# Performance work log

Hardware: AMD Instinct MI355X
Metric: run time of the kernel (lower is better)

## Reference

```python
import jax, jax.numpy as jnp
import numpy as np

TAU = 2.0          # spikingjelly LIFNode default
V_TH = 7.0         # from source
DECREASE = 0.5     # decrease_factor
ALPHA = 4.0        # sigmoid surrogate alpha (spikingjelly default)


@jax.custom_vjp
def spike(v):
    # Heaviside with sigmoid surrogate gradient
    return (v >= 0.0).astype(v.dtype)

def _spike_fwd(v):
    return spike(v), v

def _spike_bwd(v, g):
    s = jax.nn.sigmoid(ALPHA * v)
    return (g * ALPHA * s * (1.0 - s),)

spike.defvjp(_spike_fwd, _spike_bwd)


def setup_inputs() -> dict:
    key = jax.random.key(0)
    k1, k2, k3 = jax.random.split(key, 3)
    B, C, T = 4096, 14, 600
    x = jax.random.normal(k1, (B, C, T), dtype=jnp.float32)
    # weights: normal(mean=0.8, std=0.05) clamped to [0,1]; nn.Linear stores [out,in]
    W1 = jnp.clip(0.8 + 0.05 * jax.random.normal(k2, (14, 14), dtype=jnp.float32), 0.0, 1.0)
    W2 = jnp.clip(0.8 + 0.05 * jax.random.normal(k3, (500, 14), dtype=jnp.float32), 0.0, 1.0)
    return {"x": x, "W1": W1, "W2": W2}


def _forward(x, W1, W2):
    B = x.shape[0]
    xt = jnp.transpose(x, (2, 0, 1))  # [T, B, 14]

    v1_0 = jnp.zeros((B, 14), x.dtype)
    v2_0 = jnp.zeros((B, 500), x.dtype)
    cache0 = jnp.zeros((B, 14), x.dtype)

    def step(carry, x_t):
        v1, v2, cache = carry
        # block 1: linear + decayed feedback of previous spikes
        i1 = x_t @ W1.T + DECREASE * cache
        v1 = v1 + (i1 - v1) / TAU          # LIF charge (decay_input, v_reset=0)
        s1 = spike(v1 - V_TH)
        v1 = v1 * (1.0 - s1)               # hard reset to 0
        # block 2
        i2 = s1 @ W2.T
        v2 = v2 + (i2 - v2) / TAU
        s2 = spike(v2 - V_TH)
        v2 = v2 * (1.0 - s2)
        return (v1, v2, s1), None

    (v1, v2, cache), _ = jax.lax.scan(step, (v1_0, v2_0, cache0), xt)
    return jnp.exp(v2)  # liquid state [B, 500]


def reference(x, W1, W2):
    return _forward(x, W1, W2)
```

## Files before the change

### kernel.cpp

```cpp
#include <hip/hip_runtime.h>
#include <math.h>

#define T      600
#define C      14
#define NOUT   500
#define R      4
#define W      128
#define DSTR   132
#define EVCAP  256

__global__ __launch_bounds__(128, 2)
void snn_v3(const float* __restrict__ x, const float* __restrict__ W1,
            const float* __restrict__ W2, float* __restrict__ out) {
    __shared__ float    ds[R * C * DSTR];
    __shared__ unsigned evs[R * EVCAP];
    __shared__ int      ecnt[R];

    const int tid = threadIdx.x;
    const int b0  = blockIdx.x * R;
    if (tid < R) ecnt[tid] = 0;

    const int  rr   = tid >> 5;
    const int  qq   = tid & 31;
    const int  cc   = (tid >> 1) & 15;
    const int  ce   = (cc < C) ? cc : (C - 1);
    const bool aact = ((tid & 1) == 0) && (cc < C);

    float4 xv[C];
    #pragma unroll
    for (int j = 0; j < C; ++j)
        xv[j] = *(const float4*)&x[((long)(b0 + rr) * C + j) * T + qq * 4];

    float v1 = 0.f;

    for (int t0 = 0; t0 < T; t0 += W) {
        const int wlen = (T - t0 < W) ? (T - t0) : W;
        __syncthreads();

        if (qq * 4 < wlen) {
            #pragma unroll
            for (int c = 0; c < C; ++c) {
                float ax = 0.f, ay = 0.f, az = 0.f, aw = 0.f;
                #pragma unroll
                for (int j = 0; j < C; ++j) {
                    const float w = 0.5f * W1[c * C + j];
                    ax = fmaf(xv[j].x, w, ax);
                    ay = fmaf(xv[j].y, w, ay);
                    az = fmaf(xv[j].z, w, az);
                    aw = fmaf(xv[j].w, w, aw);
                }
                *(float4*)&ds[(rr * C + c) * DSTR + qq * 4] = make_float4(ax, ay, az, aw);
            }
        }

        {
            const int tn = t0 + W + qq * 4;
            if (tn < T) {
                #pragma unroll
                for (int j = 0; j < C; ++j)
                    xv[j] = *(const float4*)&x[((long)(b0 + rr) * C + j) * T + tn];
            }
        }
        __syncthreads();

        const float* dp = &ds[(rr * C + ce) * DSTR];
        for (int q = 0; q < wlen; q += 4) {
            const float4 hd = *(const float4*)&dp[q];
            const float a  = fmaf(v1, 0.5f, hd.x);
            const float b  = fmaf(a,  0.5f, hd.y);
            const float c2 = fmaf(b,  0.5f, hd.z);
            const float d  = fmaf(c2, 0.5f, hd.w);
            const float m  = fmaxf(fmaxf(a, b), fmaxf(c2, d));
            if (__builtin_expect(__ballot(m >= 7.0f) != 0ull, 0)) {
                float vv = v1;
                #pragma unroll
                for (int u = 0; u < 4; ++u) {
                    const float h = (u == 0) ? hd.x : (u == 1) ? hd.y
                                  : (u == 2) ? hd.z : hd.w;
                    vv = fmaf(vv, 0.5f, h);
                    if (vv >= 7.0f) {
                        vv = 0.5f;
                        if (aact) {
                            const int idx = atomicAdd(&ecnt[rr], 1);
                            if (idx < EVCAP)
                                evs[rr * EVCAP + idx] =
                                    ((unsigned)(t0 + q + u) << 4) | (unsigned)cc;
                        }
                    }
                }
                v1 = vv;
            } else {
                v1 = d;
            }
        }
    }
    __syncthreads();

    const int lane = tid & 31;
    const int nev  = min(ecnt[rr], EVCAP);
    const unsigned* ev = &evs[rr * EVCAP];

    float v2[16];
    #pragma unroll
    for (int k = 0; k < 16; ++k) v2[k] = 0.f;
    int tprev = -1;

    int e = 0;
    while (e < nev) {
        const int t = (int)(ev[e] >> 4);
        float i2[16];
        #pragma unroll
        for (int k = 0; k < 16; ++k) i2[k] = 0.f;
        do {
            const int c = (int)(ev[e] & 15);
            #pragma unroll
            for (int k = 0; k < 16; ++k) {
                const int o = lane + (k << 5);
                if (o < NOUT) i2[k] += W2[o * C + c];
            }
            ++e;
        } while (e < nev && (int)(ev[e] >> 4) == t);

        const int gap = t - tprev - 1;
        if (gap > 0) {
            #pragma unroll
            for (int k = 0; k < 16; ++k) v2[k] = ldexpf(v2[k], -gap);
        }
        #pragma unroll
        for (int k = 0; k < 16; ++k) {
            const float v = v2[k] + (i2[k] - v2[k]) * 0.5f;
            v2[k] = (v >= 7.0f) ? 0.f : v;
        }
        tprev = t;
    }
    {
        const int gap = (T - 1) - tprev;
        if (gap > 0) {
            #pragma unroll
            for (int k = 0; k < 16; ++k) v2[k] = ldexpf(v2[k], -gap);
        }
    }
    #pragma unroll
    for (int k = 0; k < 16; ++k) {
        const int o = lane + (k << 5);
        if (o < NOUT) out[(long)(b0 + rr) * NOUT + o] = expf(v2[k]);
    }
}

extern "C" void kernel_launch(void* const* d_in, const int* in_sizes, int n_in,
                              void* d_out, int out_size, void* d_ws, size_t ws_size,
                              hipStream_t stream) {
    const float* x  = (const float*)d_in[0];
    const float* W1 = (const float*)d_in[1];
    const float* W2 = (const float*)d_in[2];
    float* o = (float*)d_out;
    const int B = in_sizes[0] / (C * T);
    snn_v3<<<B / R, 128, 0, stream>>>(x, W1, W2, o);
}
```

Measured before the change: 44.67 us.

## Split LIF time recurrence into two parallel segments with warm-up overlap

Doubles the block to 256 threads and has each half-block run the first-layer recurrence over a different half of the time axis. The second half starts 32 steps early as a warm-up, relying on the 0.5 decay to wash out the unknown initial membrane state, and records spikes only from step 300 on. The output neurons are also split between the two halves, and each half replays both event lists. This is meant to shorten the serial critical path per block and raise occupancy, at the cost of redundant warm-up work, a per-list event cap cut to 48, and a small risk of state mismatch at the segment boundary.

```diff
diff --git a/kernel.cpp b/kernel.cpp
--- a/kernel.cpp
+++ b/kernel.cpp
@@ -5,144 +5,159 @@
 #define C      14
 #define NOUT   500
 #define R      4
-#define W      128
-#define DSTR   132
-#define EVCAP  256
+#define WW     64
+#define DSTR   68
+#define NW     6
+#define SEG1   268
+#define TMID   300
+#define CAP    48
 
-__global__ __launch_bounds__(128, 2)
-void snn_v3(const float* __restrict__ x, const float* __restrict__ W1,
+__global__ __launch_bounds__(256, 4)
+void snn_v4(const float* __restrict__ x, const float* __restrict__ W1,
             const float* __restrict__ W2, float* __restrict__ out) {
-    __shared__ float    ds[R * C * DSTR];
-    __shared__ unsigned evs[R * EVCAP];
-    __shared__ int      ecnt[R];
+    __shared__ float    ds[2 * R * C * DSTR];
+    __shared__ unsigned evs[2][R][CAP];
+    __shared__ int      ecnt[2][R];
 
     const int tid = threadIdx.x;
     const int b0  = blockIdx.x * R;
-    if (tid < R) ecnt[tid] = 0;
+    if (tid < 2 * R) ((int*)ecnt)[tid] = 0;
 
-    const int  rr   = tid >> 5;
-    const int  qq   = tid & 31;
+    const int ss = tid >> 7;
+    const int rr = (tid >> 5) & (R - 1);
+    const int qq = tid & 31;
+
+    const int wstart = ss ? SEG1 : 0;
+    const int tend   = ss ? T    : TMID;
+    const int trec   = ss ? TMID : 0;
+
     const int  cc   = (tid >> 1) & 15;
     const int  ce   = (cc < C) ? cc : (C - 1);
     const bool aact = ((tid & 1) == 0) && (cc < C);
 
-    float4 xv[C];
-    #pragma unroll
-    for (int j = 0; j < C; ++j)
-        xv[j] = *(const float4*)&x[((long)(b0 + rr) * C + j) * T + qq * 4];
-
+    float2 xv[C];
+    {
+        const int t0 = wstart + qq * 2;
+        #pragma unroll
+        for (int j = 0; j < C; ++j)
+            xv[j] = *(const float2*)&x[((long)(b0 + rr) * C + j) * T + t0];
+    }
     float v1 = 0.f;
 
-    for (int t0 = 0; t0 < T; t0 += W) {
-        const int wlen = (T - t0 < W) ? (T - t0) : W;
+    for (int w = 0; w < NW; ++w) {
+        const int tw0  = wstart + w * WW;
+        const int wlen = (tend - tw0 < WW) ? (tend - tw0) : WW;
         __syncthreads();
 
-        if (qq * 4 < wlen) {
+        if (wlen > 0) {
             #pragma unroll
             for (int c = 0; c < C; ++c) {
-                float ax = 0.f, ay = 0.f, az = 0.f, aw = 0.f;
+                float ax = 0.f, ay = 0.f;
                 #pragma unroll
                 for (int j = 0; j < C; ++j) {
-                    const float w = 0.5f * W1[c * C + j];
-                    ax = fmaf(xv[j].x, w, ax);
-                    ay = fmaf(xv[j].y, w, ay);
-                    az = fmaf(xv[j].z, w, az);
-                    aw = fmaf(xv[j].w, w, aw);
+                    const float wv = 0.5f * W1[c * C + j];
+                    ax = fmaf(xv[j].x, wv, ax);
+                    ay = fmaf(xv[j].y, wv, ay);
                 }
-                *(float4*)&ds[(rr * C + c) * DSTR + qq * 4] = make_float4(ax, ay, az, aw);
+                *(float2*)&ds[((ss * R + rr) * C + c) * DSTR + qq * 2] =
+                    make_float2(ax, ay);
             }
-        }
-
-        {
-            const int tn = t0 + W + qq * 4;
-            if (tn < T) {
-                #pragma unroll
-                for (int j = 0; j < C; ++j)
-                    xv[j] = *(const float4*)&x[((long)(b0 + rr) * C + j) * T + tn];
+            if (tw0 + WW < tend) {
+                const int tn = tw0 + WW + qq * 2;
+                if (tn + 1 < T) {
+                    #pragma unroll
+                    for (int j = 0; j < C; ++j)
+                        xv[j] = *(const float2*)&x[((long)(b0 + rr) * C + j) * T + tn];
+                }
             }
         }
         __syncthreads();
 
-        const float* dp = &ds[(rr * C + ce) * DSTR];
-        for (int q = 0; q < wlen; q += 4) {
-            const float4 hd = *(const float4*)&dp[q];
-            const float a  = fmaf(v1, 0.5f, hd.x);
-            const float b  = fmaf(a,  0.5f, hd.y);
-            const float c2 = fmaf(b,  0.5f, hd.z);
-            const float d  = fmaf(c2, 0.5f, hd.w);
-            const float m  = fmaxf(fmaxf(a, b), fmaxf(c2, d));
-            if (__builtin_expect(__ballot(m >= 7.0f) != 0ull, 0)) {
-                float vv = v1;
-                #pragma unroll
-                for (int u = 0; u < 4; ++u) {
-                    const float h = (u == 0) ? hd.x : (u == 1) ? hd.y
-                                  : (u == 2) ? hd.z : hd.w;
-                    vv = fmaf(vv, 0.5f, h);
-                    if (vv >= 7.0f) {
-                        vv = 0.5f;
-                        if (aact) {
-                            const int idx = atomicAdd(&ecnt[rr], 1);
-                            if (idx < EVCAP)
-                                evs[rr * EVCAP + idx] =
-                                    ((unsigned)(t0 + q + u) << 4) | (unsigned)cc;
+        if (wlen > 0) {
+            const float* dp = &ds[((ss * R + rr) * C + ce) * DSTR];
+            for (int q = 0; q < wlen; q += 4) {
+                const float4 hd = *(const float4*)&dp[q];
+                const float a  = fmaf(v1, 0.5f, hd.x);
+                const float b  = fmaf(a,  0.5f, hd.y);
+                const float c2 = fmaf(b,  0.5f, hd.z);
+                const float d  = fmaf(c2, 0.5f, hd.w);
+                const float m  = fmaxf(fmaxf(a, b), fmaxf(c2, d));
+                if (__builtin_expect(__ballot(m >= 7.0f) != 0ull, 0)) {
+                    float vv = v1;
+                    #pragma unroll
+                    for (int u = 0; u < 4; ++u) {
+                        const float h = (u == 0) ? hd.x : (u == 1) ? hd.y
+                                      : (u == 2) ? hd.z : hd.w;
+                        vv = fmaf(vv, 0.5f, h);
+                        if (vv >= 7.0f) {
+                            vv = 0.5f;
+                            const int t = tw0 + q + u;
+                            if (aact && t >= trec) {
+                                const int idx = atomicAdd(&ecnt[ss][rr], 1);
+                                if (idx < CAP)
+                                    evs[ss][rr][idx] =
+                                        ((unsigned)t << 4) | (unsigned)cc;
+                            }
                         }
                     }
+                    v1 = vv;
+                } else {
+                    v1 = d;
                 }
-                v1 = vv;
-            } else {
-                v1 = d;
             }
         }
     }
     __syncthreads();
 
     const int lane = tid & 31;
-    const int nev  = min(ecnt[rr], EVCAP);
-    const unsigned* ev = &evs[rr * EVCAP];
-
-    float v2[16];
+    float v2[8];
     #pragma unroll
-    for (int k = 0; k < 16; ++k) v2[k] = 0.f;
+    for (int k = 0; k < 8; ++k) v2[k] = 0.f;
     int tprev = -1;
 
-    int e = 0;
-    while (e < nev) {
-        const int t = (int)(ev[e] >> 4);
-        float i2[16];
-        #pragma unroll
-        for (int k = 0; k < 16; ++k) i2[k] = 0.f;
-        do {
-            const int c = (int)(ev[e] & 15);
+    #pragma unroll
+    for (int L = 0; L < 2; ++L) {
+        const int n = min(ecnt[L][rr], CAP);
+        const unsigned* ev = &evs[L][rr][0];
+        int e = 0;
+        while (e < n) {
+            const int t = (int)(ev[e] >> 4);
+            float i2[8];
             #pragma unroll
-            for (int k = 0; k < 16; ++k) {
-                const int o = lane + (k << 5);
-                if (o < NOUT) i2[k] += W2[o * C + c];
+            for (int k = 0; k < 8; ++k) i2[k] = 0.f;
+            do {
+                const int c = (int)(ev[e] & 15);
+                #pragma unroll
+                for (int k = 0; k < 8; ++k) {
+                    const int o = lane + ((k + 8 * ss) << 5);
+                    if (o < NOUT) i2[k] += W2[o * C + c];
+                }
+                ++e;
+            } while (e < n && (int)(ev[e] >> 4) == t);
+
+            const int gap = t - tprev - 1;
+            if (gap > 0) {
+                #pragma unroll
+                for (int k = 0; k < 8; ++k) v2[k] = ldexpf(v2[k], -gap);
             }
-            ++e;
-        } while (e < nev && (int)(ev[e] >> 4) == t);
-
-        const int gap = t - tprev - 1;
-        if (gap > 0) {
             #pragma unroll
-            for (int k = 0; k < 16; ++k) v2[k] = ldexpf(v2[k], -gap);
+            for (int k = 0; k < 8; ++k) {
+                const float v = v2[k] + (i2[k] - v2[k]) * 0.5f;
+                v2[k] = (v >= 7.0f) ? 0.f : v;
+            }
+            tprev = t;
         }
-        #pragma unroll
-        for (int k = 0; k < 16; ++k) {
-            const float v = v2[k] + (i2[k] - v2[k]) * 0.5f;
-            v2[k] = (v >= 7.0f) ? 0.f : v;
-        }
-        tprev = t;
     }
     {
         const int gap = (T - 1) - tprev;
         if (gap > 0) {
             #pragma unroll
-            for (int k = 0; k < 16; ++k) v2[k] = ldexpf(v2[k], -gap);
+            for (int k = 0; k < 8; ++k) v2[k] = ldexpf(v2[k], -gap);
         }
     }
     #pragma unroll
-    for (int k = 0; k < 16; ++k) {
-        const int o = lane + (k << 5);
+    for (int k = 0; k < 8; ++k) {
+        const int o = lane + ((k + 8 * ss) << 5);
         if (o < NOUT) out[(long)(b0 + rr) * NOUT + o] = expf(v2[k]);
     }
 }
@@ -155,5 +170,5 @@
     const float* W2 = (const float*)d_in[2];
     float* o = (float*)d_out;
     const int B = in_sizes[0] / (C * T);
-    snn_v3<<<B / R, 128, 0, stream>>>(x, W1, W2, o);
+    snn_v4<<<B / R, 256, 0, stream>>>(x, W1, W2, o);
 }
```

Result: slower. 53.65 us (+20.1%).
